# Optimization experiments

Hardware: AMD Instinct MI355X
Metric: run time of the kernel (lower is better)

Reference implementation:

```python
import jax, jax.numpy as jnp
import numpy as np

BN_EPS = 1e-5
ATT_EPS = 1e-6


def _conv(x, w, groups=1):
    # x: [B,C,H,W], w: [O, C//groups, k, k], stride 1, SAME padding for odd k
    k = w.shape[-1]
    p = (k - 1) // 2
    return jax.lax.conv_general_dilated(
        x, w, window_strides=(1, 1), padding=[(p, p), (p, p)],
        dimension_numbers=('NCHW', 'OIHW', 'NCHW'), feature_group_count=groups)


def _bn(x, bnp):
    # bnp: [4, C] stacked (scale, bias, running_mean, running_var); eval-mode BN
    s, b, m, v = bnp[0], bnp[1], bnp[2], bnp[3]
    inv = s / jnp.sqrt(v + BN_EPS)
    return x * inv[None, :, None, None] + (b - m * inv)[None, :, None, None]


def _relu6(x):
    return jnp.clip(x, 0.0, 6.0)


def _ffn(x, fc1_w, fc1_bn, conv1_w, conv1_bn, conv2_w, conv2_bn, fc2_w, fc2_bn):
    # E_FFN: 1x1 ConvBNReLU6 -> dw5x5 ConvBNReLU6 & dw3x3 ConvBNReLU6 -> sum -> 1x1 ConvBN -> ReLU6
    C = x.shape[1]
    h = _relu6(_bn(_conv(x, fc1_w), fc1_bn))
    x1 = _relu6(_bn(_conv(h, conv1_w, groups=C), conv1_bn))
    x2 = _relu6(_bn(_conv(h, conv2_w, groups=C), conv2_bn))
    return _relu6(_bn(_conv(x1 + x2, fc2_w), fc2_bn))


def _bias(y, b):
    return y + b[None, :, None, None]


def setup_inputs() -> dict:
    key = jax.random.key(0)
    ks = jax.random.split(key, 16)
    C, M = 64, 8  # in_places, in_places // scale
    B, H, W = 4, 224, 224

    def w(k, shape, s=0.05):
        return (jax.random.normal(k, shape, dtype=jnp.float32) * s)

    def bn_params(k, c):
        k1, k2, k3, k4 = jax.random.split(k, 4)
        scale = 1.0 + 0.1 * jax.random.normal(k1, (c,), dtype=jnp.float32)
        bias = 0.1 * jax.random.normal(k2, (c,), dtype=jnp.float32)
        mean = 0.1 * jax.random.normal(k3, (c,), dtype=jnp.float32)
        var = 1.0 + 0.1 * jax.random.uniform(k4, (c,), dtype=jnp.float32)
        return jnp.stack([scale, bias, mean, var])  # [4, c]

    return {
        'x': jax.random.normal(ks[0], (B, C, H, W), dtype=jnp.float32),
        'gamma': jnp.full((1,), 0.5, dtype=jnp.float32),  # nonzero so attention branch matters
        'q_w': w(ks[1], (M, C, 1, 1)), 'q_b': w(ks[2], (M,)),
        'k_w': w(ks[3], (M, C, 1, 1)), 'k_b': w(ks[4], (M,)),
        'v_w': w(ks[5], (C, C, 1, 1)), 'v_b': w(ks[6], (C,)),
        'fc1_w': w(ks[7], (C, C, 1, 1)), 'fc1_bn': bn_params(ks[8], C),
        'conv1_w': w(ks[9], (C, 1, 5, 5)), 'conv1_bn': bn_params(ks[10], C),
        'conv2_w': w(ks[11], (C, 1, 3, 3)), 'conv2_bn': bn_params(ks[12], C),
        'fc2_w': w(ks[13], (C, C, 1, 1)), 'fc2_bn': bn_params(ks[14], C),
    }


def reference(x, gamma, q_w, q_b, k_w, k_b, v_w, v_b,
              fc1_w, fc1_bn, conv1_w, conv1_bn, conv2_w, conv2_bn, fc2_w, fc2_bn):
    B, C, H, W = x.shape
    N = H * W
    x_channel = _ffn(x, fc1_w, fc1_bn, conv1_w, conv1_bn, conv2_w, conv2_bn, fc2_w, fc2_bn)
    # softplus feature maps; Q,K: [B, m, N]
    Q = jax.nn.softplus(_bias(_conv(x, q_w), q_b).reshape(B, -1, N))
    K = jax.nn.softplus(_bias(_conv(x, k_w), k_b).reshape(B, -1, N))
    V = (_bias(_conv(x, v_w), v_b) + x_channel).reshape(B, C, N)
    Qt = jnp.swapaxes(Q, 1, 2)                              # [B, N, m]
    KV = jnp.einsum('bmn,bcn->bmc', K, V)                   # [B, m, C]
    norm = 1.0 / jnp.einsum('bnm,bm->bn', Qt, K.sum(-1) + ATT_EPS)  # [B, N]
    wv = jnp.einsum('bnm,bmc,bn->bcn', Qt, KV, norm).reshape(B, C, H, W)
    return x + gamma * wv
```

## Files before the change

### kernel.cpp

```cpp
#include <hip/hip_runtime.h>
#include <math.h>

#define B_ 4
#define C_ 64
#define M_ 8
#define H_ 224
#define W_ 224
#define N_ (H_*W_)
#define CN_ (C_*N_)
#define MN_ (M_*N_)
#define BCN_ (B_*CN_)
#define BMN_ (B_*MN_)

__device__ __forceinline__ float relu6f(float v){ return fminf(fmaxf(v,0.0f),6.0f); }
__device__ __forceinline__ float softplusf(float v){
  return v > 0.0f ? v + log1pf(expf(-v)) : log1pf(expf(v));
}

#define FMA4(A, W, X) { A.x = fmaf((W), (X).x, A.x); A.y = fmaf((W), (X).y, A.y); \
                        A.z = fmaf((W), (X).z, A.z); A.w = fmaf((W), (X).w, A.w); }

__global__ __launch_bounds__(256) void k_fc1k(const float* __restrict__ x,
                                              const float* __restrict__ w,
                                              const float* __restrict__ bn,
                                              const float* __restrict__ kw,
                                              const float* __restrict__ kb,
                                              float* __restrict__ h,
                                              float* __restrict__ Kq)
{
  __shared__ float xsl[2*1024];
  __shared__ float wl [2*512];
  __shared__ float kt [512];
  const int tid  = threadIdx.x;
  const int b    = blockIdx.x / 392;
  const int pg   = blockIdx.x % 392;
  const int pix0 = pg*128;
  const float* xb = x + (size_t)b*CN_ + pix0;

  for (int idx = tid; idx < 512; idx += 256) {
    const int c = idx >> 3, m = idx & 7;
    kt[idx] = kw[m*64 + c];
  }

  const int scp = tid >> 5;
  const int spx = (tid & 31) << 2;
  const int e0 = tid*2, e1 = tid*2+1;
  const int wc0 = e0 >> 6, wo0 = e0 & 63;
  const int wc1 = e1 >> 6, wo1 = e1 & 63;

  {
    const float4 xr = *(const float4*)(xb + (size_t)scp*N_ + spx);
    const float w0r = w[wo0*64 + wc0];
    const float w1r = w[wo1*64 + wc1];
    *(float4*)&xsl[scp*128 + spx] = xr;
    wl[e0] = w0r; wl[e1] = w1r;
  }
  __syncthreads();

  const int lane = tid & 63, wv_ = tid >> 6;
  const int och  = 2*wv_ + (lane >> 5);
  const int ocb  = och*8;
  const int px4  = (lane & 31) << 2;

  float4 ah[8];
  float4 ak = {0,0,0,0};
  #pragma unroll
  for (int i = 0; i < 8; ++i) ah[i] = make_float4(0.f,0.f,0.f,0.f);

  for (int ck = 0; ck < 8; ++ck) {
    const int cur = ck & 1, nxt = cur ^ 1;
    const float* xc = &xsl[cur*1024];
    const float* wc = &wl[cur*512];
    float4 xr; float w0r, w1r;
    if (ck < 7) {
      const int c0n = (ck+1)*8;
      xr  = *(const float4*)(xb + (size_t)(c0n + scp)*N_ + spx);
      w0r = w[wo0*64 + c0n + wc0];
      w1r = w[wo1*64 + c0n + wc1];
    }
    #pragma unroll
    for (int cp = 0; cp < 8; ++cp) {
      const float4 xv = *(const float4*)&xc[cp*128 + px4];
      const float4 w0 = *(const float4*)&wc[cp*64 + ocb];
      const float4 w1 = *(const float4*)&wc[cp*64 + ocb + 4];
      const float kvw = kt[(ck*8+cp)*8 + och];
      FMA4(ah[0], w0.x, xv); FMA4(ah[1], w0.y, xv);
      FMA4(ah[2], w0.z, xv); FMA4(ah[3], w0.w, xv);
      FMA4(ah[4], w1.x, xv); FMA4(ah[5], w1.y, xv);
      FMA4(ah[6], w1.z, xv); FMA4(ah[7], w1.w, xv);
      FMA4(ak, kvw, xv);
    }
    if (ck < 7) {
      *(float4*)&xsl[nxt*1024 + scp*128 + spx] = xr;
      wl[nxt*512 + e0] = w0r; wl[nxt*512 + e1] = w1r;
    }
    __syncthreads();
  }

  float* hb = h + (size_t)b*CN_ + pix0 + px4;
  #pragma unroll
  for (int o = 0; o < 8; ++o) {
    const int oc = ocb + o;
    const float inv  = bn[oc] / sqrtf(bn[192+oc] + 1e-5f);
    const float beta = bn[64+oc] - bn[128+oc]*inv;
    float4 o4;
    o4.x = relu6f(fmaf(ah[o].x, inv, beta));
    o4.y = relu6f(fmaf(ah[o].y, inv, beta));
    o4.z = relu6f(fmaf(ah[o].z, inv, beta));
    o4.w = relu6f(fmaf(ah[o].w, inv, beta));
    *(float4*)(hb + (size_t)oc*N_) = o4;
  }
  {
    const float kbm = kb[och];
    float4 q;
    q.x = softplusf(ak.x + kbm); q.y = softplusf(ak.y + kbm);
    q.z = softplusf(ak.z + kbm); q.w = softplusf(ak.w + kbm);
    *(float4*)(Kq + (size_t)b*MN_ + (size_t)och*N_ + pix0 + px4) = q;
  }
}

__global__ __launch_bounds__(256) void k_dw(const float* __restrict__ h,
                                            const float* __restrict__ w5,
                                            const float* __restrict__ w3,
                                            const float* __restrict__ bn1,
                                            const float* __restrict__ bn2,
                                            float* __restrict__ s)
{
  __shared__ float tile[36*37];
  const int tid = threadIdx.x;
  const int blk = blockIdx.x;
  const int t   = blk % 49;
  const int bc  = blk / 49;
  const int c   = bc & 63;
  const int tx0 = (t % 7) * 32;
  const int ty0 = (t / 7) * 32;
  const float* hb = h + (size_t)bc * N_;

  for (int idx = tid; idx < 1296; idx += 256) {
    const int ly = idx / 36, lx = idx - ly*36;
    const int gy = ty0 + ly - 2, gx = tx0 + lx - 2;
    float v = 0.0f;
    if (gy >= 0 && gy < H_ && gx >= 0 && gx < W_) v = hb[gy*W_ + gx];
    tile[ly*37 + lx] = v;
  }
  __syncthreads();

  float w5r[25], w3r[9];
  #pragma unroll
  for (int i = 0; i < 25; ++i) w5r[i] = w5[c*25 + i];
  #pragma unroll
  for (int i = 0; i < 9; ++i)  w3r[i] = w3[c*9 + i];
  const float inv1 = bn1[c] / sqrtf(bn1[192+c] + 1e-5f);
  const float bet1 = bn1[64+c] - bn1[128+c]*inv1;
  const float inv2 = bn2[c] / sqrtf(bn2[192+c] + 1e-5f);
  const float bet2 = bn2[64+c] - bn2[128+c]*inv2;

  const int ty  = tid >> 3;
  const int tx4 = (tid & 7) << 2;
  float a5[4] = {0,0,0,0}, a3[4] = {0,0,0,0};
  #pragma unroll
  for (int dy = 0; dy < 5; ++dy) {
    float r[8];
    #pragma unroll
    for (int i = 0; i < 8; ++i) r[i] = tile[(ty+dy)*37 + tx4 + i];
    #pragma unroll
    for (int dx = 0; dx < 5; ++dx) {
      const float wv = w5r[dy*5+dx];
      #pragma unroll
      for (int p = 0; p < 4; ++p) a5[p] = fmaf(wv, r[p+dx], a5[p]);
    }
    if (dy >= 1 && dy <= 3) {
      #pragma unroll
      for (int dx = 1; dx <= 3; ++dx) {
        const float wv = w3r[(dy-1)*3+(dx-1)];
        #pragma unroll
        for (int p = 0; p < 4; ++p) a3[p] = fmaf(wv, r[p+dx], a3[p]);
      }
    }
  }
  float* sb = s + (size_t)bc * N_ + (ty0+ty)*W_ + tx0 + tx4;
  float4 o4;
  o4.x = relu6f(fmaf(a5[0],inv1,bet1)) + relu6f(fmaf(a3[0],inv2,bet2));
  o4.y = relu6f(fmaf(a5[1],inv1,bet1)) + relu6f(fmaf(a3[1],inv2,bet2));
  o4.z = relu6f(fmaf(a5[2],inv1,bet1)) + relu6f(fmaf(a3[2],inv2,bet2));
  o4.w = relu6f(fmaf(a5[3],inv1,bet1)) + relu6f(fmaf(a3[3],inv2,bet2));
  *(float4*)sb = o4;
}

__global__ __launch_bounds__(256) void k_v(const float* __restrict__ x,
                                           const float* __restrict__ s,
                                           const float* __restrict__ vw,
                                           const float* __restrict__ vb,
                                           const float* __restrict__ fw,
                                           const float* __restrict__ fbn,
                                           float* __restrict__ V)
{
  __shared__ float xsl[2*1024];
  __shared__ float ssl[2*1024];
  __shared__ float wvl[2*512];
  __shared__ float wfl[2*512];
  const int tid  = threadIdx.x;
  const int b    = blockIdx.x / 392;
  const int pg   = blockIdx.x % 392;
  const int pix0 = pg*128;
  const float* xb = x + (size_t)b*CN_ + pix0;
  const float* sb = s + (size_t)b*CN_ + pix0;

  const int scp = tid >> 5;
  const int spx = (tid & 31) << 2;
  const int e0 = tid*2, e1 = tid*2+1;
  const int wc0 = e0 >> 6, wo0 = e0 & 63;
  const int wc1 = e1 >> 6, wo1 = e1 & 63;

  {
    const float4 xr = *(const float4*)(xb + (size_t)scp*N_ + spx);
    const float4 sr = *(const float4*)(sb + (size_t)scp*N_ + spx);
    const float a0 = vw[wo0*64 + wc0], a1 = vw[wo1*64 + wc1];
    const float f0 = fw[wo0*64 + wc0], f1 = fw[wo1*64 + wc1];
    *(float4*)&xsl[scp*128 + spx] = xr;
    *(float4*)&ssl[scp*128 + spx] = sr;
    wvl[e0] = a0; wvl[e1] = a1;
    wfl[e0] = f0; wfl[e1] = f1;
  }
  __syncthreads();

  const int lane = tid & 63, wv_ = tid >> 6;
  const int och  = 2*wv_ + (lane >> 5);
  const int ocb  = och*8;
  const int px4  = (lane & 31) << 2;

  float4 av[8], af[8];
  #pragma unroll
  for (int i = 0; i < 8; ++i) { av[i] = make_float4(0,0,0,0); af[i] = make_float4(0,0,0,0); }

  for (int ck = 0; ck < 8; ++ck) {
    const int cur = ck & 1, nxt = cur ^ 1;
    const float* xc = &xsl[cur*1024];
    const float* sc2 = &ssl[cur*1024];
    const float* wvc = &wvl[cur*512];
    const float* wfc = &wfl[cur*512];
    float4 xr, sr; float a0r, a1r, f0r, f1r;
    if (ck < 7) {
      const int c0n = (ck+1)*8;
      xr  = *(const float4*)(xb + (size_t)(c0n + scp)*N_ + spx);
      sr  = *(const float4*)(sb + (size_t)(c0n + scp)*N_ + spx);
      a0r = vw[wo0*64 + c0n + wc0]; a1r = vw[wo1*64 + c0n + wc1];
      f0r = fw[wo0*64 + c0n + wc0]; f1r = fw[wo1*64 + c0n + wc1];
    }
    #pragma unroll
    for (int cp = 0; cp < 8; ++cp) {
      const float4 xv = *(const float4*)&xc[cp*128 + px4];
      const float4 sv = *(const float4*)&sc2[cp*128 + px4];
      const float4 wa0 = *(const float4*)&wvc[cp*64 + ocb];
      const float4 wa1 = *(const float4*)&wvc[cp*64 + ocb + 4];
      const float4 wf0 = *(const float4*)&wfc[cp*64 + ocb];
      const float4 wf1 = *(const float4*)&wfc[cp*64 + ocb + 4];
      FMA4(av[0], wa0.x, xv); FMA4(av[1], wa0.y, xv);
      FMA4(av[2], wa0.z, xv); FMA4(av[3], wa0.w, xv);
      FMA4(av[4], wa1.x, xv); FMA4(av[5], wa1.y, xv);
      FMA4(av[6], wa1.z, xv); FMA4(av[7], wa1.w, xv);
      FMA4(af[0], wf0.x, sv); FMA4(af[1], wf0.y, sv);
      FMA4(af[2], wf0.z, sv); FMA4(af[3], wf0.w, sv);
      FMA4(af[4], wf1.x, sv); FMA4(af[5], wf1.y, sv);
      FMA4(af[6], wf1.z, sv); FMA4(af[7], wf1.w, sv);
    }
    if (ck < 7) {
      *(float4*)&xsl[nxt*1024 + scp*128 + spx] = xr;
      *(float4*)&ssl[nxt*1024 + scp*128 + spx] = sr;
      wvl[nxt*512 + e0] = a0r; wvl[nxt*512 + e1] = a1r;
      wfl[nxt*512 + e0] = f0r; wfl[nxt*512 + e1] = f1r;
    }
    __syncthreads();
  }

  float* Vb = V + (size_t)b*CN_ + pix0 + px4;
  #pragma unroll
  for (int o = 0; o < 8; ++o) {
    const int oc = ocb + o;
    const float inv  = fbn[oc] / sqrtf(fbn[192+oc] + 1e-5f);
    const float beta = fbn[64+oc] - fbn[128+oc]*inv;
    const float bias = vb[oc];
    float4 o4;
    o4.x = av[o].x + bias + relu6f(fmaf(af[o].x, inv, beta));
    o4.y = av[o].y + bias + relu6f(fmaf(af[o].y, inv, beta));
    o4.z = av[o].z + bias + relu6f(fmaf(af[o].z, inv, beta));
    o4.w = av[o].w + bias + relu6f(fmaf(af[o].w, inv, beta));
    *(float4*)(Vb + (size_t)oc*N_) = o4;
  }
}

__global__ __launch_bounds__(256) void k_kv(const float* __restrict__ V,
                                            const float* __restrict__ Kq,
                                            float* __restrict__ KV,
                                            float* __restrict__ Ksum)
{
  const int blk = blockIdx.x;
  const int b   = blk >> 7;
  const int rem = blk & 127;
  const int cg  = rem >> 4;
  const int ch  = rem & 15;
  const int tid = threadIdx.x;
  const int base = ch * 3136;
  const int end  = base + 3136;
  const float* Kb = Kq + (size_t)b*MN_;
  const float* Vb = V  + (size_t)b*CN_ + (size_t)(cg*8)*N_;

  float acc[64];
  #pragma unroll
  for (int i = 0; i < 64; ++i) acc[i] = 0.0f;
  float ks[8] = {0,0,0,0,0,0,0,0};

  for (int n4 = base + tid*4; n4 < end; n4 += 1024) {
    float4 kr[8];
    #pragma unroll
    for (int m2 = 0; m2 < 8; ++m2) kr[m2] = *(const float4*)(Kb + (size_t)m2*N_ + n4);
    #pragma unroll
    for (int m2 = 0; m2 < 8; ++m2)
      ks[m2] += (kr[m2].x + kr[m2].y) + (kr[m2].z + kr[m2].w);
    #pragma unroll
    for (int c8 = 0; c8 < 8; ++c8) {
      const float4 vv = *(const float4*)(Vb + (size_t)c8*N_ + n4);
      #pragma unroll
      for (int m2 = 0; m2 < 8; ++m2) {
        float t = acc[m2*8+c8];
        t = fmaf(kr[m2].x, vv.x, t);
        t = fmaf(kr[m2].y, vv.y, t);
        t = fmaf(kr[m2].z, vv.z, t);
        t = fmaf(kr[m2].w, vv.w, t);
        acc[m2*8+c8] = t;
      }
    }
  }
  const int lane = tid & 63;

  {
    int nv = 64;
    #pragma unroll
    for (int mask = 1; mask <= 32; mask <<= 1) {
      nv >>= 1;
      const bool hi = (lane & mask) != 0;
      #pragma unroll
      for (int i = 0; i < 32; ++i) {
        if (i < nv) {
          const float mine = hi ? acc[i] : acc[i+nv];
          const float th = __shfl_xor(mine, mask);
          acc[i] = (hi ? acc[i+nv] : acc[i]) + th;
        }
      }
    }
  }
  const int j = 32*(lane & 1) + 16*((lane >> 1) & 1) + 8*((lane >> 2) & 1)
              + 4*((lane >> 3) & 1) + 2*((lane >> 4) & 1) + ((lane >> 5) & 1);
  atomicAdd(&KV[b*512 + (j >> 3)*64 + cg*8 + (j & 7)], acc[0]);

  if (cg == 0) {
    float mk = 0.0f;
    #pragma unroll
    for (int jj = 0; jj < 8; ++jj) {
      float v = ks[jj];
      v += __shfl_xor(v, 1);
      v += __shfl_xor(v, 2);
      v += __shfl_xor(v, 4);
      v += __shfl_xor(v, 8);
      v += __shfl_xor(v, 16);
      v += __shfl_xor(v, 32);
      if (lane == jj) mk = v;
    }
    if (lane < 8) atomicAdd(&Ksum[b*8 + lane], mk);
  }
}

__global__ __launch_bounds__(256) void k_out(const float* __restrict__ x,
                                             const float* __restrict__ qw,
                                             const float* __restrict__ qb,
                                             const float* __restrict__ gamma,
                                             const float* __restrict__ KV,
                                             const float* __restrict__ Ksum,
                                             float* __restrict__ out)
{
  __shared__ float xs[64*128];
  __shared__ __align__(16) float kvt[64*8];
  __shared__ __align__(16) float qwt[64*8];
  __shared__ float qs[8][128];
  __shared__ float scl[128];
  __shared__ float ksl[8];
  const int tid = threadIdx.x;
  const int b  = blockIdx.x / 392;
  const int pg = blockIdx.x % 392;
  const int pix0 = pg*128;
  const float* xb = x + (size_t)b*CN_ + pix0;

  for (int idx = tid; idx < 512; idx += 256) {
    const int m = idx >> 6, c = idx & 63;
    kvt[c*8 + m] = KV[b*512 + idx];
    qwt[c*8 + m] = qw[idx];
  }
  if (tid < 8) ksl[tid] = Ksum[b*8 + tid] + 1e-6f;
  #pragma unroll
  for (int i = 0; i < 8; ++i) {
    const int idx = i*256 + tid;
    const int c = idx >> 5, p4 = (idx & 31) << 2;
    const float4 v = *(const float4*)(xb + (size_t)c*N_ + p4);
    *(float4*)&xs[c*128 + p4] = v;
  }
  __syncthreads();

  if (tid < 128) {
    const int px = tid;
    float q[8] = {0,0,0,0,0,0,0,0};
    #pragma unroll 8
    for (int c = 0; c < 64; ++c) {
      const float xv = xs[c*128 + px];
      const float4 w0 = *(const float4*)&qwt[c*8];
      const float4 w1 = *(const float4*)&qwt[c*8+4];
      q[0] = fmaf(w0.x, xv, q[0]);
      q[1] = fmaf(w0.y, xv, q[1]);
      q[2] = fmaf(w0.z, xv, q[2]);
      q[3] = fmaf(w0.w, xv, q[3]);
      q[4] = fmaf(w1.x, xv, q[4]);
      q[5] = fmaf(w1.y, xv, q[5]);
      q[6] = fmaf(w1.z, xv, q[6]);
      q[7] = fmaf(w1.w, xv, q[7]);
    }
    float den = 0.0f;
    #pragma unroll
    for (int m = 0; m < 8; ++m) {
      q[m] = softplusf(q[m] + qb[m]);
      den  = fmaf(q[m], ksl[m], den);
      qs[m][px] = q[m];
    }
    scl[px] = gamma[0] / den;
  }
  __syncthreads();

  float* ob = out + (size_t)b*CN_ + pix0;
  #pragma unroll
  for (int i = 0; i < 32; ++i) {
    const int idx = i*256 + tid;
    const int c = idx >> 7, px = idx & 127;
    const float4 k0 = *(const float4*)&kvt[c*8];
    const float4 k1 = *(const float4*)&kvt[c*8+4];
    float wv;
    wv = qs[0][px]*k0.x;
    wv = fmaf(qs[1][px], k0.y, wv);
    wv = fmaf(qs[2][px], k0.z, wv);
    wv = fmaf(qs[3][px], k0.w, wv);
    wv = fmaf(qs[4][px], k1.x, wv);
    wv = fmaf(qs[5][px], k1.y, wv);
    wv = fmaf(qs[6][px], k1.z, wv);
    wv = fmaf(qs[7][px], k1.w, wv);
    ob[(size_t)c*N_ + px] = fmaf(scl[px], wv, xs[c*128 + px]);
  }
}

extern "C" void kernel_launch(void* const* d_in, const int* in_sizes, int n_in,
                              void* d_out, int out_size, void* d_ws, size_t ws_size,
                              hipStream_t stream) {
  const float* x      = (const float*)d_in[0];
  const float* gamma  = (const float*)d_in[1];
  const float* q_w    = (const float*)d_in[2];
  const float* q_b    = (const float*)d_in[3];
  const float* k_w    = (const float*)d_in[4];
  const float* k_b    = (const float*)d_in[5];
  const float* v_w    = (const float*)d_in[6];
  const float* v_b    = (const float*)d_in[7];
  const float* fc1_w  = (const float*)d_in[8];
  const float* fc1_bn = (const float*)d_in[9];
  const float* c1_w   = (const float*)d_in[10];
  const float* c1_bn  = (const float*)d_in[11];
  const float* c2_w   = (const float*)d_in[12];
  const float* c2_bn  = (const float*)d_in[13];
  const float* fc2_w  = (const float*)d_in[14];
  const float* fc2_bn = (const float*)d_in[15];
  float* outp = (float*)d_out;

  float* ws   = (float*)d_ws;
  float* bufA = ws;
  float* bufS = ws + (size_t)BCN_;
  float* bufK = ws + (size_t)2*BCN_;
  float* kv   = ws + (size_t)2*BCN_ + BMN_;
  float* ksum = kv + 2048;

  hipMemsetAsync(kv, 0, (2048 + 32)*sizeof(float), stream);

  k_fc1k<<<dim3(B_*392), dim3(256), 0, stream>>>(x, fc1_w, fc1_bn, k_w, k_b, bufA, bufK);
  k_dw  <<<dim3(B_*C_*49), dim3(256), 0, stream>>>(bufA, c1_w, c2_w, c1_bn, c2_bn, bufS);
  k_v   <<<dim3(B_*392), dim3(256), 0, stream>>>(x, bufS, v_w, v_b, fc2_w, fc2_bn, bufA);
  k_kv  <<<dim3(512), dim3(256), 0, stream>>>(bufA, bufK, kv, ksum);
  k_out <<<dim3(B_*392), dim3(256), 0, stream>>>(x, q_w, q_b, gamma, kv, ksum, outp);
}
```

Measured before the change: 315.2 us.

## Use bf16 MFMA for fused v-projection and fc2 1x1 convolutions

Rewrites the k_v kernel so the two 64x64 pointwise convolutions (v projection on x and fc2 on the summed depthwise output) run on bf16 MFMA 16x16x32 instructions instead of scalar FP32 FMAs. Inputs are converted to bf16 and staged in shared memory in one pass, replacing the double-buffered FP32 channel pipeline, and BN/bias constants are precomputed into shared memory. This cuts ALU work for the matmuls but lowers precision to bf16. It also adds strided 2-byte LDS gathers and scalar 4-byte output stores in place of float4 stores.

```diff
diff --git a/kernel.cpp b/kernel.cpp
--- a/kernel.cpp
+++ b/kernel.cpp
@@ -12,9 +12,18 @@
 #define BCN_ (B_*CN_)
 #define BMN_ (B_*MN_)
 
+typedef __attribute__((ext_vector_type(8))) short short8;
+typedef __attribute__((ext_vector_type(4))) float f32x4;
+typedef __attribute__((ext_vector_type(4))) unsigned int uint4v;
+
 __device__ __forceinline__ float relu6f(float v){ return fminf(fmaxf(v,0.0f),6.0f); }
 __device__ __forceinline__ float softplusf(float v){
   return v > 0.0f ? v + log1pf(expf(-v)) : log1pf(expf(v));
+}
+__device__ __forceinline__ unsigned int rne2(float lo, float hi){
+  unsigned int ul = __float_as_uint(lo); ul += 0x7FFFu + ((ul>>16)&1u);
+  unsigned int uh = __float_as_uint(hi); uh += 0x7FFFu + ((uh>>16)&1u);
+  return (ul>>16) | (uh & 0xFFFF0000u);
 }
 
 #define FMA4(A, W, X) { A.x = fmaf((W), (X).x, A.x); A.y = fmaf((W), (X).y, A.y); \
@@ -187,6 +196,23 @@
   *(float4*)sb = o4;
 }
 
+__device__ __forceinline__ short8 bfrag(const unsigned short* __restrict__ L,
+                                        int px, int c0){
+  const unsigned short* p = L + c0*128 + px;
+  unsigned int w0 = (unsigned int)p[0]   | ((unsigned int)p[128]<<16);
+  unsigned int w1 = (unsigned int)p[256] | ((unsigned int)p[384]<<16);
+  unsigned int w2 = (unsigned int)p[512] | ((unsigned int)p[640]<<16);
+  unsigned int w3 = (unsigned int)p[768] | ((unsigned int)p[896]<<16);
+  uint4v q = {w0,w1,w2,w3};
+  return __builtin_bit_cast(short8, q);
+}
+__device__ __forceinline__ short8 afrag(const float* __restrict__ W, int idx){
+  const float4 f0 = *(const float4*)(W + idx);
+  const float4 f1 = *(const float4*)(W + idx + 4);
+  uint4v q = {rne2(f0.x,f0.y), rne2(f0.z,f0.w), rne2(f1.x,f1.y), rne2(f1.z,f1.w)};
+  return __builtin_bit_cast(short8, q);
+}
+
 __global__ __launch_bounds__(256) void k_v(const float* __restrict__ x,
                                            const float* __restrict__ s,
                                            const float* __restrict__ vw,
@@ -195,10 +221,9 @@
                                            const float* __restrict__ fbn,
                                            float* __restrict__ V)
 {
-  __shared__ float xsl[2*1024];
-  __shared__ float ssl[2*1024];
-  __shared__ float wvl[2*512];
-  __shared__ float wfl[2*512];
+  __shared__ unsigned short xls[64*128];
+  __shared__ unsigned short sls[64*128];
+  __shared__ float invb[3][64];
   const int tid  = threadIdx.x;
   const int b    = blockIdx.x / 392;
   const int pg   = blockIdx.x % 392;
@@ -208,84 +233,79 @@
 
   const int scp = tid >> 5;
   const int spx = (tid & 31) << 2;
-  const int e0 = tid*2, e1 = tid*2+1;
-  const int wc0 = e0 >> 6, wo0 = e0 & 63;
-  const int wc1 = e1 >> 6, wo1 = e1 & 63;
-
-  {
-    const float4 xr = *(const float4*)(xb + (size_t)scp*N_ + spx);
-    const float4 sr = *(const float4*)(sb + (size_t)scp*N_ + spx);
-    const float a0 = vw[wo0*64 + wc0], a1 = vw[wo1*64 + wc1];
-    const float f0 = fw[wo0*64 + wc0], f1 = fw[wo1*64 + wc1];
-    *(float4*)&xsl[scp*128 + spx] = xr;
-    *(float4*)&ssl[scp*128 + spx] = sr;
-    wvl[e0] = a0; wvl[e1] = a1;
-    wfl[e0] = f0; wfl[e1] = f1;
+  #pragma unroll
+  for (int i = 0; i < 8; ++i) {
+    const int c = i*8 + scp;
+    const float4 xr = *(const float4*)(xb + (size_t)c*N_ + spx);
+    const float4 sr = *(const float4*)(sb + (size_t)c*N_ + spx);
+    *(uint2*)&xls[c*128 + spx] = make_uint2(rne2(xr.x,xr.y), rne2(xr.z,xr.w));
+    *(uint2*)&sls[c*128 + spx] = make_uint2(rne2(sr.x,sr.y), rne2(sr.z,sr.w));
+  }
+  if (tid < 64) {
+    const float inv = fbn[tid] / sqrtf(fbn[192+tid] + 1e-5f);
+    invb[0][tid] = inv;
+    invb[1][tid] = fbn[64+tid] - fbn[128+tid]*inv;
+    invb[2][tid] = vb[tid];
   }
   __syncthreads();
 
-  const int lane = tid & 63, wv_ = tid >> 6;
-  const int och  = 2*wv_ + (lane >> 5);
-  const int ocb  = och*8;
-  const int px4  = (lane & 31) << 2;
-
-  float4 av[8], af[8];
-  #pragma unroll
-  for (int i = 0; i < 8; ++i) { av[i] = make_float4(0,0,0,0); af[i] = make_float4(0,0,0,0); }
-
-  for (int ck = 0; ck < 8; ++ck) {
-    const int cur = ck & 1, nxt = cur ^ 1;
-    const float* xc = &xsl[cur*1024];
-    const float* sc2 = &ssl[cur*1024];
-    const float* wvc = &wvl[cur*512];
-    const float* wfc = &wfl[cur*512];
-    float4 xr, sr; float a0r, a1r, f0r, f1r;
-    if (ck < 7) {
-      const int c0n = (ck+1)*8;
-      xr  = *(const float4*)(xb + (size_t)(c0n + scp)*N_ + spx);
-      sr  = *(const float4*)(sb + (size_t)(c0n + scp)*N_ + spx);
-      a0r = vw[wo0*64 + c0n + wc0]; a1r = vw[wo1*64 + c0n + wc1];
-      f0r = fw[wo0*64 + c0n + wc0]; f1r = fw[wo1*64 + c0n + wc1];
-    }
-    #pragma unroll
-    for (int cp = 0; cp < 8; ++cp) {
-      const float4 xv = *(const float4*)&xc[cp*128 + px4];
-      const float4 sv = *(const float4*)&sc2[cp*128 + px4];
-      const float4 wa0 = *(const float4*)&wvc[cp*64 + ocb];
-      const float4 wa1 = *(const float4*)&wvc[cp*64 + ocb + 4];
-      const float4 wf0 = *(const float4*)&wfc[cp*64 + ocb];
-      const float4 wf1 = *(const float4*)&wfc[cp*64 + ocb + 4];
-      FMA4(av[0], wa0.x, xv); FMA4(av[1], wa0.y, xv);
-      FMA4(av[2], wa0.z, xv); FMA4(av[3], wa0.w, xv);
-      FMA4(av[4], wa1.x, xv); FMA4(av[5], wa1.y, xv);
-      FMA4(av[6], wa1.z, xv); FMA4(av[7], wa1.w, xv);
-      FMA4(af[0], wf0.x, sv); FMA4(af[1], wf0.y, sv);
-      FMA4(af[2], wf0.z, sv); FMA4(af[3], wf0.w, sv);
-      FMA4(af[4], wf1.x, sv); FMA4(af[5], wf1.y, sv);
-      FMA4(af[6], wf1.z, sv); FMA4(af[7], wf1.w, sv);
-    }
-    if (ck < 7) {
-      *(float4*)&xsl[nxt*1024 + scp*128 + spx] = xr;
-      *(float4*)&ssl[nxt*1024 + scp*128 + spx] = sr;
-      wvl[nxt*512 + e0] = a0r; wvl[nxt*512 + e1] = a1r;
-      wfl[nxt*512 + e0] = f0r; wfl[nxt*512 + e1] = f1r;
-    }
-    __syncthreads();
-  }
-
-  float* Vb = V + (size_t)b*CN_ + pix0 + px4;
-  #pragma unroll
-  for (int o = 0; o < 8; ++o) {
-    const int oc = ocb + o;
-    const float inv  = fbn[oc] / sqrtf(fbn[192+oc] + 1e-5f);
-    const float beta = fbn[64+oc] - fbn[128+oc]*inv;
-    const float bias = vb[oc];
-    float4 o4;
-    o4.x = av[o].x + bias + relu6f(fmaf(af[o].x, inv, beta));
-    o4.y = av[o].y + bias + relu6f(fmaf(af[o].y, inv, beta));
-    o4.z = av[o].z + bias + relu6f(fmaf(af[o].z, inv, beta));
-    o4.w = av[o].w + bias + relu6f(fmaf(af[o].w, inv, beta));
-    *(float4*)(Vb + (size_t)oc*N_) = o4;
+  const int lane = tid & 63, wv = tid >> 6;
+  const int l15 = lane & 15, u = lane >> 4;
+  const int pxw = wv*32;
+
+  f32x4 av[4][2], af[4][2];
+  #pragma unroll
+  for (int t = 0; t < 4; ++t)
+    #pragma unroll
+    for (int s2 = 0; s2 < 2; ++s2) { av[t][s2] = (f32x4){0.f,0.f,0.f,0.f};
+                                     af[t][s2] = (f32x4){0.f,0.f,0.f,0.f}; }
+
+  #pragma unroll
+  for (int kk = 0; kk < 2; ++kk) {
+    const int c0 = kk*32 + u*8;
+    {
+      const short8 a0 = afrag(vw, (0*16+l15)*64 + c0);
+      const short8 a1 = afrag(vw, (1*16+l15)*64 + c0);
+      const short8 a2 = afrag(vw, (2*16+l15)*64 + c0);
+      const short8 a3 = afrag(vw, (3*16+l15)*64 + c0);
+      #pragma unroll
+      for (int s2 = 0; s2 < 2; ++s2) {
+        const short8 bx = bfrag(xls, pxw + s2*16 + l15, c0);
+        av[0][s2] = __builtin_amdgcn_mfma_f32_16x16x32_bf16(a0, bx, av[0][s2], 0,0,0);
+        av[1][s2] = __builtin_amdgcn_mfma_f32_16x16x32_bf16(a1, bx, av[1][s2], 0,0,0);
+        av[2][s2] = __builtin_amdgcn_mfma_f32_16x16x32_bf16(a2, bx, av[2][s2], 0,0,0);
+        av[3][s2] = __builtin_amdgcn_mfma_f32_16x16x32_bf16(a3, bx, av[3][s2], 0,0,0);
+      }
+    }
+    {
+      const short8 a0 = afrag(fw, (0*16+l15)*64 + c0);
+      const short8 a1 = afrag(fw, (1*16+l15)*64 + c0);
+      const short8 a2 = afrag(fw, (2*16+l15)*64 + c0);
+      const short8 a3 = afrag(fw, (3*16+l15)*64 + c0);
+      #pragma unroll
+      for (int s2 = 0; s2 < 2; ++s2) {
+        const short8 bs = bfrag(sls, pxw + s2*16 + l15, c0);
+        af[0][s2] = __builtin_amdgcn_mfma_f32_16x16x32_bf16(a0, bs, af[0][s2], 0,0,0);
+        af[1][s2] = __builtin_amdgcn_mfma_f32_16x16x32_bf16(a1, bs, af[1][s2], 0,0,0);
+        af[2][s2] = __builtin_amdgcn_mfma_f32_16x16x32_bf16(a2, bs, af[2][s2], 0,0,0);
+        af[3][s2] = __builtin_amdgcn_mfma_f32_16x16x32_bf16(a3, bs, af[3][s2], 0,0,0);
+      }
+    }
+  }
+
+  float* Vb = V + (size_t)b*CN_ + pix0;
+  #pragma unroll
+  for (int t = 0; t < 4; ++t) {
+    #pragma unroll
+    for (int s2 = 0; s2 < 2; ++s2) {
+      const int px = pxw + s2*16 + l15;
+      #pragma unroll
+      for (int r = 0; r < 4; ++r) {
+        const int oc = t*16 + u*4 + r;
+        Vb[(size_t)oc*N_ + px] = av[t][s2][r] + invb[2][oc]
+            + relu6f(fmaf(af[t][s2][r], invb[0][oc], invb[1][oc]));
+      }
+    }
   }
 }
 
```

After: 302.4 us. 1.04x faster.
